# Kernel tuning notes

Measured on AMD Instinct MI355X. Metric: run time of the kernel, lower is better.

Reference implementation:

```python
import jax, jax.numpy as jnp
import numpy as np

IN_CH = 4096
OUT_CH = 11008
W_BITS = 4


def unpack_weight(qweight, wbit):
    # qweight: [in_ch * wbit // 32, out_ch] int32 -> intweight: [in_ch, out_ch] int32
    rows, cols = qweight.shape
    n = rows * (32 // wbit)
    i = jnp.arange(n)
    idx = (i * wbit) // 32            # which packed word each row comes from
    off = (i * wbit) % 32             # bit offset within the word
    # wbit=4 divides 32, so every value lies inside one word (simple path only)
    shift = (32 - off - wbit).astype(jnp.int32)
    mask = jnp.int32((1 << wbit) - 1)
    return jnp.bitwise_and(jnp.right_shift(qweight[idx], shift[:, None]), mask)


def setup_inputs() -> dict:
    key = jax.random.key(0)
    k1, k2, k3, k4 = jax.random.split(key, 4)
    x = jax.random.normal(k1, (4, 2048, IN_CH), dtype=jnp.float32)
    pack_weight = jax.random.randint(k2, (IN_CH * W_BITS // 32, OUT_CH), 0, 2**31 - 1, dtype=jnp.int32)
    w_scale = jax.random.uniform(k3, (OUT_CH, 1), dtype=jnp.float32) * 0.01 + 1e-3
    w_zero_point = jax.random.uniform(k4, (OUT_CH, 1), dtype=jnp.float32) * 15.0
    return {"x": x, "pack_weight": pack_weight, "w_scale": w_scale, "w_zero_point": w_zero_point}


def reference(x, pack_weight, w_scale, w_zero_point):
    # unpack int4 -> [in, out], transpose to [out, in] like w.t() in torch
    intw = unpack_weight(pack_weight, W_BITS).T.astype(x.dtype)  # [out, in]
    # per-channel dequant: scale/zero are [out, 1]
    w = (intw - w_zero_point) * w_scale                          # [out, in]
    # F.linear(x, w): x @ w.T
    return jnp.einsum('bsi,oi->bso', x, w)
```

## Files before the change

### kernel.cpp

```cpp
#include <hip/hip_runtime.h>
#include <hip/hip_bf16.h>


#define K_DIM 4096
#define N_DIM 11008
#define M_DIM 8192
#define NTILE (K_DIM / 64)

typedef unsigned short u16;
typedef __attribute__((ext_vector_type(8))) short short8;
typedef __attribute__((ext_vector_type(4))) float f32x4;
typedef __attribute__((ext_vector_type(4))) unsigned int u32x4;

__device__ __forceinline__ unsigned cvt2(float a, float b) {
    __hip_bfloat162 h = __float22bfloat162_rn(make_float2(a, b));
    unsigned u;
    __builtin_memcpy(&u, &h, 4);
    return u;
}

#define GLOAD_LDS16(g, l)                                                 \
    __builtin_amdgcn_global_load_lds(                                     \
        (const __attribute__((address_space(1))) unsigned int*)(g),       \
        (__attribute__((address_space(3))) unsigned int*)(l), 16, 0, 0)

__global__ __launch_bounds__(256) void xcvt(const float* __restrict__ X,
                                            u16* __restrict__ Xb) {
    const size_t i = ((size_t)blockIdx.x * 256 + threadIdx.x) * 8;
    f32x4 a = *(const f32x4*)(X + i);
    f32x4 b = *(const f32x4*)(X + i + 4);
    u32x4 v;
    v[0] = cvt2(a[0], a[1]);
    v[1] = cvt2(a[2], a[3]);
    v[2] = cvt2(b[0], b[1]);
    v[3] = cvt2(b[2], b[3]);
    *(u32x4*)(Xb + i) = v;
}

__global__ __launch_bounds__(256) void wdeq(const int* __restrict__ Q,
                                            const float* __restrict__ SC,
                                            const float* __restrict__ ZP,
                                            u16* __restrict__ Wt) {
    const int t  = threadIdx.x;
    const int n  = blockIdx.x * 32 + (t >> 3);
    const int kw = blockIdx.y * 8 + (t & 7);
    const unsigned w = (unsigned)Q[(size_t)kw * N_DIM + n];
    const float sc  = SC[n];
    const float nzs = -ZP[n] * sc;
    float f[8];
#pragma unroll
    for (int j = 0; j < 8; ++j)
        f[j] = fmaf((float)((w >> (28 - 4 * j)) & 15u), sc, nzs);
    u32x4 v;
    v[0] = cvt2(f[0], f[1]);
    v[1] = cvt2(f[2], f[3]);
    v[2] = cvt2(f[4], f[5]);
    v[3] = cvt2(f[6], f[7]);
    *(u32x4*)(Wt + (size_t)n * K_DIM + kw * 8) = v;
}

__global__ __launch_bounds__(512, 2) void qgemm_8ph(const u16* __restrict__ Ab,
                                                    const u16* __restrict__ Bt,
                                                    float* __restrict__ C) {
    __shared__ u16 lds[8 * 8192];

    const int tid  = threadIdx.x;
    const int lane = tid & 63;
    const int wave = tid >> 6;
    const int wm = wave >> 2;
    const int wn = wave & 3;

    const int bid = (int)blockIdx.x;
    const int swz = (bid & 7) * 172 + (bid >> 3);
    const int bx = swz % 43;
    const int by = swz / 43;
    const int m0 = by * 256;
    const int n0 = bx * 256;

    const int srow = tid >> 2;
    const int sg   = (tid & 3) ^ ((tid >> 3) & 3);
    const u16* gA = Ab + (size_t)(m0 + srow) * K_DIM + sg * 8;
    const u16* gB = Bt + (size_t)(n0 + srow) * K_DIM + sg * 8;
    u16* ldst = &lds[tid * 8];

    auto stage = [&](int buf, int mat, int kh, int kt) {
        const u16* g = (mat ? gB : gA) + kt * 64 + kh * 32;
        u16* l = ldst + ((buf * 2 + mat) * 2 + kh) * 8192;
        GLOAD_LDS16(g, l);
        GLOAD_LDS16(g + (size_t)128 * K_DIM, l + 4096);
    };

    const int fr = lane & 15;
    const int fq = lane >> 4;
    const int uo = (fq ^ ((fr >> 1) & 3)) * 8;
    const int aoff = (wm * 128 + fr) * 32 + uo;
    const int boff = (wn * 64 + fr) * 32 + uo;

    short8 af[4], bf[4];
    f32x4 acc[8][4] = {};

    auto rdA = [&](int buf, int kh, int half) {
        const u16* p = &lds[(buf * 4 + kh) * 8192 + aoff + half * 2048];
#pragma unroll
        for (int i = 0; i < 4; ++i) af[i] = *(const short8*)(p + i * 512);
    };
    auto rdB = [&](int buf, int kh) {
        const u16* p = &lds[((buf * 2 + 1) * 2 + kh) * 8192 + boff];
#pragma unroll
        for (int i = 0; i < 4; ++i) bf[i] = *(const short8*)(p + i * 512);
    };
    auto quad = [&](int half) {
        __builtin_amdgcn_s_setprio(1);
#pragma unroll
        for (int mi = 0; mi < 4; ++mi)
#pragma unroll
            for (int ni = 0; ni < 4; ++ni)
                acc[half * 4 + mi][ni] = __builtin_amdgcn_mfma_f32_16x16x32_bf16(
                    af[mi], bf[ni], acc[half * 4 + mi][ni], 0, 0, 0);
        __builtin_amdgcn_s_setprio(0);
    };

    stage(0, 0, 0, 0); stage(0, 1, 0, 0); stage(0, 0, 1, 0); stage(0, 1, 1, 0);
    stage(1, 0, 0, 1); stage(1, 1, 0, 1);
    asm volatile("s_waitcnt vmcnt(4)" ::: "memory");
    __builtin_amdgcn_s_barrier();

    for (int T = 0; T < NTILE; ++T) {
        const int b = T & 1;
        const bool p1 = (T + 1 < NTILE);
        const bool p2 = (T + 2 < NTILE);

        rdA(b, 0, 0); rdB(b, 0);
        if (p1) stage(b ^ 1, 0, 1, T + 1);
        __builtin_amdgcn_s_barrier();
        quad(0);
        __builtin_amdgcn_s_barrier();

        rdA(b, 0, 1);
        if (p1) stage(b ^ 1, 1, 1, T + 1);
        __builtin_amdgcn_s_barrier();
        quad(1);
        __builtin_amdgcn_s_barrier();

        rdA(b, 1, 0); rdB(b, 1);
        if (p2) stage(b, 0, 0, T + 2);
        __builtin_amdgcn_s_barrier();
        quad(0);
        __builtin_amdgcn_s_barrier();

        rdA(b, 1, 1);
        if (p2) {
            stage(b, 1, 0, T + 2);
            asm volatile("s_waitcnt vmcnt(4)" ::: "memory");
        } else if (p1) {
            asm volatile("s_waitcnt vmcnt(0)" ::: "memory");
        }
        __builtin_amdgcn_s_barrier();
        quad(1);
        __builtin_amdgcn_s_barrier();
    }

#pragma unroll
    for (int mf = 0; mf < 8; ++mf) {
#pragma unroll
        for (int ni = 0; ni < 4; ++ni) {
            const int row = m0 + wm * 128 + mf * 16 + fq * 4;
            const int col = n0 + wn * 64 + ni * 16 + fr;
            float* cp = C + (size_t)row * N_DIM + col;
#pragma unroll
            for (int r = 0; r < 4; ++r)
                cp[(size_t)r * N_DIM] = acc[mf][ni][r];
        }
    }
}

#define LDA 40
__global__ __launch_bounds__(256, 3) void qgemm_fused(
    const float* __restrict__ X, const int* __restrict__ Q,
    const float* __restrict__ SC, const float* __restrict__ ZP,
    float* __restrict__ C)
{
    __shared__ short As[128 * LDA];
    __shared__ short Bs[128 * LDA];

    const int tid  = threadIdx.x;
    const int lane = tid & 63;
    const int wave = tid >> 6;

    const int m0 = blockIdx.y * 128;
    const int n0 = blockIdx.x * 128;

    const int arow = tid >> 2;
    const int ak8  = (tid & 3) * 8;
    const float* xbase = X + (size_t)(m0 + arow) * K_DIM + ak8;

    const int bcol  = tid & 127;
    const int brow0 = tid >> 7;
    const int* qbase = Q + (size_t)brow0 * N_DIM + n0 + bcol;
    const float sc  = SC[n0 + bcol];
    const float nzs = -ZP[n0 + bcol] * sc;

    f32x4 areg[4];
    int   breg[2];

    auto load_tile = [&](int kt) {
        const float* p0 = xbase + kt;
        areg[0] = *(const f32x4*)(p0);
        areg[1] = *(const f32x4*)(p0 + 4);
        const float* p1 = p0 + (size_t)64 * K_DIM;
        areg[2] = *(const f32x4*)(p1);
        areg[3] = *(const f32x4*)(p1 + 4);
        const int* q0 = qbase + (size_t)(kt >> 3) * N_DIM;
        breg[0] = q0[0];
        breg[1] = q0[2 * N_DIM];
    };

    auto store_tile = [&]() {
        #pragma unroll
        for (int p = 0; p < 2; ++p) {
            u32x4 v;
            v[0] = cvt2(areg[2*p+0][0], areg[2*p+0][1]);
            v[1] = cvt2(areg[2*p+0][2], areg[2*p+0][3]);
            v[2] = cvt2(areg[2*p+1][0], areg[2*p+1][1]);
            v[3] = cvt2(areg[2*p+1][2], areg[2*p+1][3]);
            *(u32x4*)&As[(arow + p * 64) * LDA + ak8] = v;
        }
        #pragma unroll
        for (int r = 0; r < 2; ++r) {
            const unsigned w = (unsigned)breg[r];
            float f[8];
            #pragma unroll
            for (int j = 0; j < 8; ++j)
                f[j] = fmaf((float)((w >> (28 - 4*j)) & 15u), sc, nzs);
            u32x4 v;
            v[0] = cvt2(f[0], f[1]);
            v[1] = cvt2(f[2], f[3]);
            v[2] = cvt2(f[4], f[5]);
            v[3] = cvt2(f[6], f[7]);
            *(u32x4*)&Bs[bcol * LDA + (brow0 + 2*r) * 8] = v;
        }
    };

    f32x4 acc[4][4] = {};

    const int wm = (wave >> 1) * 64;
    const int wn = (wave & 1) * 64;
    const int fr = lane & 15;
    const int fq = lane >> 4;

    const short* Abase = &As[(wm + fr) * LDA + fq * 8];
    const short* Bbase = &Bs[(wn + fr) * LDA + fq * 8];

    load_tile(0);
    store_tile();
    __syncthreads();

    for (int kt = 0;;) {
        const int knext = kt + 32;
        const bool last = (knext >= K_DIM);
        if (!last) load_tile(knext);

        short8 af[4], bf[4];
        #pragma unroll
        for (int i = 0; i < 4; ++i) {
            af[i] = *(const short8*)(Abase + i * 16 * LDA);
            bf[i] = *(const short8*)(Bbase + i * 16 * LDA);
        }
        #pragma unroll
        for (int mi = 0; mi < 4; ++mi)
            #pragma unroll
            for (int ni = 0; ni < 4; ++ni)
                acc[mi][ni] = __builtin_amdgcn_mfma_f32_16x16x32_bf16(
                    af[mi], bf[ni], acc[mi][ni], 0, 0, 0);

        if (last) break;
        __syncthreads();
        store_tile();
        __syncthreads();
        kt = knext;
    }

    #pragma unroll
    for (int mi = 0; mi < 4; ++mi) {
        #pragma unroll
        for (int ni = 0; ni < 4; ++ni) {
            const int row = m0 + wm + mi * 16 + fq * 4;
            const int col = n0 + wn + ni * 16 + fr;
            float* cp = C + (size_t)row * N_DIM + col;
            #pragma unroll
            for (int r = 0; r < 4; ++r)
                cp[(size_t)r * N_DIM] = acc[mi][ni][r];
        }
    }
}

extern "C" void kernel_launch(void* const* d_in, const int* in_sizes, int n_in,
                              void* d_out, int out_size, void* d_ws, size_t ws_size,
                              hipStream_t stream) {
    const float* X  = (const float*)d_in[0];
    const int*   Q  = (const int*)d_in[1];
    const float* SC = (const float*)d_in[2];
    const float* ZP = (const float*)d_in[3];
    float*       C  = (float*)d_out;
    (void)in_sizes; (void)n_in; (void)out_size;

    const size_t xb_bytes = (size_t)M_DIM * K_DIM * 2;
    const size_t wt_bytes = (size_t)N_DIM * K_DIM * 2;

    if (ws_size >= xb_bytes + wt_bytes) {
        u16* Xb = (u16*)d_ws;
        u16* Wt = (u16*)((char*)d_ws + xb_bytes);
        xcvt<<<dim3(M_DIM * K_DIM / (256 * 8)), 256, 0, stream>>>(X, Xb);
        wdeq<<<dim3(N_DIM / 32, K_DIM / 64), 256, 0, stream>>>(Q, SC, ZP, Wt);
        qgemm_8ph<<<dim3((N_DIM / 256) * (M_DIM / 256)), 512, 0, stream>>>(Xb, Wt, C);
    } else {
        qgemm_fused<<<dim3(N_DIM / 128, M_DIM / 128), 256, 0, stream>>>(X, Q, SC, ZP, C);
    }
}
```

Baseline: 1.135 ms.

## Switch bf16 GEMM to 32x32x16 MFMA and halve per-tile phase count

```diff
diff --git a/kernel.cpp b/kernel.cpp
--- a/kernel.cpp
+++ b/kernel.cpp
@@ -10,6 +10,7 @@
 typedef unsigned short u16;
 typedef __attribute__((ext_vector_type(8))) short short8;
 typedef __attribute__((ext_vector_type(4))) float f32x4;
+typedef __attribute__((ext_vector_type(16))) float f32x16;
 typedef __attribute__((ext_vector_type(4))) unsigned int u32x4;
 
 __device__ __forceinline__ unsigned cvt2(float a, float b) {
@@ -59,9 +60,9 @@
     *(u32x4*)(Wt + (size_t)n * K_DIM + kw * 8) = v;
 }
 
-__global__ __launch_bounds__(512, 2) void qgemm_8ph(const u16* __restrict__ Ab,
-                                                    const u16* __restrict__ Bt,
-                                                    float* __restrict__ C) {
+__global__ __launch_bounds__(512, 2) void qgemm_32(const u16* __restrict__ Ab,
+                                                   const u16* __restrict__ Bt,
+                                                   float* __restrict__ C) {
     __shared__ u16 lds[8 * 8192];
 
     const int tid  = threadIdx.x;
@@ -90,33 +91,39 @@
         GLOAD_LDS16(g + (size_t)128 * K_DIM, l + 4096);
     };
 
-    const int fr = lane & 15;
-    const int fq = lane >> 4;
-    const int uo = (fq ^ ((fr >> 1) & 3)) * 8;
-    const int aoff = (wm * 128 + fr) * 32 + uo;
-    const int boff = (wn * 64 + fr) * 32 + uo;
-
-    short8 af[4], bf[4];
-    f32x4 acc[8][4] = {};
-
-    auto rdA = [&](int buf, int kh, int half) {
-        const u16* p = &lds[(buf * 4 + kh) * 8192 + aoff + half * 2048];
-#pragma unroll
-        for (int i = 0; i < 4; ++i) af[i] = *(const short8*)(p + i * 512);
-    };
-    auto rdB = [&](int buf, int kh) {
-        const u16* p = &lds[((buf * 2 + 1) * 2 + kh) * 8192 + boff];
-#pragma unroll
-        for (int i = 0; i < 4; ++i) bf[i] = *(const short8*)(p + i * 512);
-    };
-    auto quad = [&](int half) {
+    const int c31 = lane & 31;
+    const int hi  = lane >> 5;
+    const int sw  = (c31 >> 1) & 3;
+    const int arow0 = (wm * 128 + c31) * 32;
+    const int brow0 = (wn * 64 + c31) * 32;
+
+    short8 af[2][4], bf[2][2];
+    f32x16 acc[4][2] = {};
+
+    auto rdAB = [&](int buf, int kh) {
+        const u16* pa = &lds[(buf * 4 + kh) * 8192];
+        const u16* pb = &lds[(buf * 4 + 2 + kh) * 8192];
+#pragma unroll
+        for (int s = 0; s < 2; ++s) {
+            const int uo = ((2 * s + hi) ^ sw) * 8;
+#pragma unroll
+            for (int mi = 0; mi < 4; ++mi)
+                af[s][mi] = *(const short8*)(pa + arow0 + mi * 1024 + uo);
+#pragma unroll
+            for (int ni = 0; ni < 2; ++ni)
+                bf[s][ni] = *(const short8*)(pb + brow0 + ni * 1024 + uo);
+        }
+    };
+    auto mmac = [&]() {
         __builtin_amdgcn_s_setprio(1);
 #pragma unroll
-        for (int mi = 0; mi < 4; ++mi)
-#pragma unroll
-            for (int ni = 0; ni < 4; ++ni)
-                acc[half * 4 + mi][ni] = __builtin_amdgcn_mfma_f32_16x16x32_bf16(
-                    af[mi], bf[ni], acc[half * 4 + mi][ni], 0, 0, 0);
+        for (int s = 0; s < 2; ++s)
+#pragma unroll
+            for (int mi = 0; mi < 4; ++mi)
+#pragma unroll
+                for (int ni = 0; ni < 2; ++ni)
+                    acc[mi][ni] = __builtin_amdgcn_mfma_f32_32x32x16_bf16(
+                        af[s][mi], bf[s][ni], acc[mi][ni], 0, 0, 0);
         __builtin_amdgcn_s_setprio(0);
     };
 
@@ -130,46 +137,35 @@
         const bool p1 = (T + 1 < NTILE);
         const bool p2 = (T + 2 < NTILE);
 
-        rdA(b, 0, 0); rdB(b, 0);
-        if (p1) stage(b ^ 1, 0, 1, T + 1);
+        rdAB(b, 0);
+        if (p1) { stage(b ^ 1, 0, 1, T + 1); stage(b ^ 1, 1, 1, T + 1); }
         __builtin_amdgcn_s_barrier();
-        quad(0);
+        mmac();
         __builtin_amdgcn_s_barrier();
 
-        rdA(b, 0, 1);
-        if (p1) stage(b ^ 1, 1, 1, T + 1);
-        __builtin_amdgcn_s_barrier();
-        quad(1);
-        __builtin_amdgcn_s_barrier();
-
-        rdA(b, 1, 0); rdB(b, 1);
-        if (p2) stage(b, 0, 0, T + 2);
-        __builtin_amdgcn_s_barrier();
-        quad(0);
-        __builtin_amdgcn_s_barrier();
-
-        rdA(b, 1, 1);
+        rdAB(b, 1);
         if (p2) {
-            stage(b, 1, 0, T + 2);
+            stage(b, 0, 0, T + 2); stage(b, 1, 0, T + 2);
             asm volatile("s_waitcnt vmcnt(4)" ::: "memory");
         } else if (p1) {
             asm volatile("s_waitcnt vmcnt(0)" ::: "memory");
         }
         __builtin_amdgcn_s_barrier();
-        quad(1);
+        mmac();
         __builtin_amdgcn_s_barrier();
     }
 
 #pragma unroll
-    for (int mf = 0; mf < 8; ++mf) {
-#pragma unroll
-        for (int ni = 0; ni < 4; ++ni) {
-            const int row = m0 + wm * 128 + mf * 16 + fq * 4;
-            const int col = n0 + wn * 64 + ni * 16 + fr;
-            float* cp = C + (size_t)row * N_DIM + col;
-#pragma unroll
-            for (int r = 0; r < 4; ++r)
-                cp[(size_t)r * N_DIM] = acc[mf][ni][r];
+    for (int mi = 0; mi < 4; ++mi) {
+#pragma unroll
+        for (int ni = 0; ni < 2; ++ni) {
+            const int rbase = m0 + wm * 128 + mi * 32 + 4 * hi;
+            const int col   = n0 + wn * 64 + ni * 32 + c31;
+#pragma unroll
+            for (int r = 0; r < 16; ++r) {
+                const int row = rbase + (r & 3) + 8 * (r >> 2);
+                C[(size_t)row * N_DIM + col] = acc[mi][ni][r];
+            }
         }
     }
 }
@@ -312,7 +308,7 @@
         u16* Wt = (u16*)((char*)d_ws + xb_bytes);
         xcvt<<<dim3(M_DIM * K_DIM / (256 * 8)), 256, 0, stream>>>(X, Xb);
         wdeq<<<dim3(N_DIM / 32, K_DIM / 64), 256, 0, stream>>>(Q, SC, ZP, Wt);
-        qgemm_8ph<<<dim3((N_DIM / 256) * (M_DIM / 256)), 512, 0, stream>>>(Xb, Wt, C);
+        qgemm_32<<<dim3((N_DIM / 256) * (M_DIM / 256)), 512, 0, stream>>>(Xb, Wt, C);
     } else {
         qgemm_fused<<<dim3(N_DIM / 128, M_DIM / 128), 256, 0, stream>>>(X, Q, SC, ZP, C);
     }
```

Result: slower. 1.218 ms (+7.3%).
